# Kernel optimization log

Measured on AMD Instinct MI355X. Metric: run time of the kernel, lower is better.

Reference implementation:

```python
import jax, jax.numpy as jnp
import numpy as np

B, H, W, C = 32, 512, 512, 3


def setup_inputs() -> dict:
    key = jax.random.key(0)
    k1, k2, k3 = jax.random.split(key, 3)
    images = jax.random.normal(k1, (B, H, W, C), dtype=jnp.float32)
    # focal lengths in pixels, positive and well-conditioned
    focal = 400.0 + 200.0 * jax.random.uniform(k2, (B, 2), dtype=jnp.float32)
    # quaternion ~ identity rotation + small noise (stddev=0.01), q0 mean 1
    q = jnp.array([1.0, 0.0, 0.0, 0.0], jnp.float32) + 0.01 * jax.random.normal(k3, (4,), dtype=jnp.float32)
    return {"images": images, "focal": focal, "q": q}


def _quaternion_to_R(q):
    # matches tf_quaternion_to_R: normalize so sum(q^2)=2, then outer product
    q = q * jnp.sqrt(2.0 / jnp.sum(q * q))
    Q = q[:, None] * q[None, :]  # [4,4], Q[i,j] = q_i q_j
    return jnp.array([
        [1.0 - Q[2, 2] - Q[3, 3], Q[1, 2] - Q[3, 0], Q[1, 3] + Q[2, 0]],
        [Q[1, 2] + Q[3, 0], 1.0 - Q[1, 1] - Q[3, 3], Q[2, 3] - Q[1, 0]],
        [Q[1, 3] - Q[2, 0], Q[2, 3] + Q[1, 0], 1.0 - Q[1, 1] - Q[2, 2]],
    ])


def _forward(images, focal, q):
    R = _quaternion_to_R(q)  # [3,3]
    d = jnp.concatenate([focal, jnp.ones((focal.shape[0], 1), focal.dtype)], axis=1)  # [B,3]
    # H = K @ R @ inv(K) with K = diag(d):  H[b,i,j] = d[b,i] * R[i,j] / d[b,j]
    Hm = R[None, :, :] * d[:, :, None] / d[:, None, :]  # [B,3,3]

    origin_x = jnp.float32(W / 2)
    origin_y = jnp.float32(H / 2)
    xs = jnp.arange(W, dtype=jnp.float32) - origin_x  # [W]
    ys = jnp.arange(H, dtype=jnp.float32) - origin_y  # [H]
    x, y = jnp.meshgrid(xs, ys)  # [H,W] each
    ps = jnp.stack([x.ravel(), y.ravel(), jnp.ones(H * W, jnp.float32)], axis=0)  # [3,N]

    ps_w = jnp.einsum('bij,jn->bin', Hm, ps)  # [B,3,N]
    x_w = (ps_w[:, 0, :] / ps_w[:, 2, :]).reshape(-1, H, W) + origin_x  # [B,H,W]
    y_w = (ps_w[:, 1, :] / ps_w[:, 2, :]).reshape(-1, H, W) + origin_y  # [B,H,W]

    # bilinear resampler (tf.contrib.resampler): zero outside image bounds
    x0 = jnp.floor(x_w)
    y0 = jnp.floor(y_w)
    wx = x_w - x0
    wy = y_w - y0
    x0i = x0.astype(jnp.int32)
    y0i = y0.astype(jnp.int32)

    b = jnp.arange(images.shape[0])[:, None, None]

    def corner(yi, xi, w):
        valid = (xi >= 0) & (xi <= W - 1) & (yi >= 0) & (yi <= H - 1)
        g = images[b, jnp.clip(yi, 0, H - 1), jnp.clip(xi, 0, W - 1)]  # [B,H,W,C]
        return g * (w * valid.astype(images.dtype))[..., None]

    out = (corner(y0i, x0i, (1.0 - wx) * (1.0 - wy))
           + corner(y0i, x0i + 1, wx * (1.0 - wy))
           + corner(y0i + 1, x0i, (1.0 - wx) * wy)
           + corner(y0i + 1, x0i + 1, wx * wy))
    return out


def reference(images, focal, q):
    return _forward(images, focal, q)
```

## Files before the change

### kernel.cpp

```cpp
#include <hip/hip_runtime.h>
#include <hip/hip_bf16.h>


#define IMG_H 512
#define IMG_W 512
#define IMG_C 3
#define NB    32

typedef float f32x4  __attribute__((ext_vector_type(4)));
typedef float f32x4u __attribute__((ext_vector_type(4), aligned(4)));
typedef float f32x2u __attribute__((ext_vector_type(2), aligned(4)));

__global__ __launch_bounds__(256) void warp_kernel(
    const float* __restrict__ images,
    const float* __restrict__ focal,
    const float* __restrict__ q,
    float* __restrict__ out)
{
    const unsigned bid  = blockIdx.x;
    const unsigned xcd  = bid & 7u;
    const unsigned slot = bid >> 3;
    const unsigned virt = xcd * 2048u + slot;
    const int b = (int)(virt >> 9);
    const int y = (int)(virt & 511u);

    const int tid = threadIdx.x;

    __shared__ float sH[9];
    __shared__ float s_out[IMG_W * IMG_C];

    if (tid == 0) {
        float q0 = q[0], q1 = q[1], q2 = q[2], q3 = q[3];
        float s = sqrtf(2.0f / (q0*q0 + q1*q1 + q2*q2 + q3*q3));
        q0 *= s; q1 *= s; q2 *= s; q3 *= s;
        float R00 = 1.0f - q2*q2 - q3*q3;
        float R01 = q1*q2 - q3*q0;
        float R02 = q1*q3 + q2*q0;
        float R10 = q1*q2 + q3*q0;
        float R11 = 1.0f - q1*q1 - q3*q3;
        float R12 = q2*q3 - q1*q0;
        float R20 = q1*q3 - q2*q0;
        float R21 = q2*q3 + q1*q0;
        float R22 = 1.0f - q1*q1 - q2*q2;
        float d0 = focal[b*2 + 0];
        float d1 = focal[b*2 + 1];
        sH[0] = (R00*d0)/d0; sH[1] = (R01*d0)/d1; sH[2] = (R02*d0);
        sH[3] = (R10*d1)/d0; sH[4] = (R11*d1)/d1; sH[5] = (R12*d1);
        sH[6] = R20/d0;      sH[7] = R21/d1;      sH[8] = R22;
    }
    __syncthreads();

    const float h0 = sH[0], h3 = sH[3], h6 = sH[6];

    const float ys = (float)y - 256.0f;
    const float r1 = sH[1]*ys + sH[2];
    const float r4 = sH[4]*ys + sH[5];
    const float r7 = sH[7]*ys + sH[8];

    const float* __restrict__ img_b = images + (unsigned)b * (IMG_H * IMG_W * IMG_C);

    #define SAMPLE(PX, A0, A1, A2) do {                                        \
        const float xs = (float)(PX) - 256.0f;                                 \
        float p0 = fmaf(h0, xs, r1);                                           \
        float p1 = fmaf(h3, xs, r4);                                           \
        float p2 = fmaf(h6, xs, r7);                                           \
        float rp2 = __builtin_amdgcn_rcpf(p2);                                 \
        float xw = fmaf(p0, rp2, 256.0f);                                      \
        float yw = fmaf(p1, rp2, 256.0f);                                      \
        float x0f = floorf(xw), y0f = floorf(yw);                              \
        float wx = xw - x0f,   wy = yw - y0f;                                  \
        int x0 = (int)x0f, y0i = (int)y0f;                                     \
        bool interior = (x0 >= 0) & (y0i >= 0) &                               \
                        (x0 < IMG_W-1) & (y0i < IMG_H-1);                      \
        if (__all(interior)) {                                                 \
             \
            const float* bpA = img_b + ((unsigned)y0i * IMG_W + (unsigned)x0) * 3u; \
            const float* bpB = bpA + IMG_W * 3u;                               \
            f32x4u vA0 = *reinterpret_cast<const f32x4u*>(bpA);                \
            f32x2u vA1 = *reinterpret_cast<const f32x2u*>(bpA + 4);            \
            f32x4u vB0 = *reinterpret_cast<const f32x4u*>(bpB);                \
            f32x2u vB1 = *reinterpret_cast<const f32x2u*>(bpB + 4);            \
            float w00 = (1.0f - wx) * (1.0f - wy);                             \
            float w01 = wx * (1.0f - wy);                                      \
            float w10 = (1.0f - wx) * wy;                                      \
            float w11 = wx * wy;                                               \
            A0 = vA0.x*w00 + vA0.w*w01 + vB0.x*w10 + vB0.w*w11;                \
            A1 = vA0.y*w00 + vA1.x*w01 + vB0.y*w10 + vB1.x*w11;                \
            A2 = vA0.z*w00 + vA1.y*w01 + vB0.z*w10 + vB1.y*w11;                \
        } else {                                                               \
                     \
            int x1 = x0 + 1, y1i = y0i + 1;                                    \
            bool vx0 = (x0 >= 0) & (x0 <= IMG_W-1);                            \
            bool vx1 = (x1 >= 0) & (x1 <= IMG_W-1);                            \
            bool vy0 = (y0i >= 0) & (y0i <= IMG_H-1);                          \
            bool vy1 = (y1i >= 0) & (y1i <= IMG_H-1);                          \
            unsigned xc0 = (unsigned)min(max(x0, 0), IMG_W-1);                 \
            unsigned xc1 = (unsigned)min(max(x1, 0), IMG_W-1);                 \
            unsigned yc0 = (unsigned)min(max(y0i, 0), IMG_H-1);                \
            unsigned yc1 = (unsigned)min(max(y1i, 0), IMG_H-1);                \
            const float* p00 = img_b + (yc0 * IMG_W + xc0) * IMG_C;            \
            const float* p01 = img_b + (yc0 * IMG_W + xc1) * IMG_C;            \
            const float* p10 = img_b + (yc1 * IMG_W + xc0) * IMG_C;            \
            const float* p11 = img_b + (yc1 * IMG_W + xc1) * IMG_C;            \
            float a00 = p00[0], a01 = p00[1], a02 = p00[2];                    \
            float b00 = p01[0], b01 = p01[1], b02 = p01[2];                    \
            float c00 = p10[0], c01 = p10[1], c02 = p10[2];                    \
            float d00 = p11[0], d01 = p11[1], d02 = p11[2];                    \
            float w00 = (vx0 & vy0) ? (1.0f - wx) * (1.0f - wy) : 0.0f;        \
            float w01 = (vx1 & vy0) ? wx * (1.0f - wy)          : 0.0f;        \
            float w10 = (vx0 & vy1) ? (1.0f - wx) * wy          : 0.0f;        \
            float w11 = (vx1 & vy1) ? wx * wy                   : 0.0f;        \
            A0 = a00*w00 + b00*w01 + c00*w10 + d00*w11;                        \
            A1 = a01*w00 + b01*w01 + c01*w10 + d01*w11;                        \
            A2 = a02*w00 + b02*w01 + c02*w10 + d02*w11;                        \
        }                                                                      \
    } while (0)

    float o0a, o1a, o2a, o0b, o1b, o2b;
    SAMPLE(tid,        o0a, o1a, o2a);
    SAMPLE(tid + 256,  o0b, o1b, o2b);
    #undef SAMPLE

    s_out[tid*3 + 0] = o0a;
    s_out[tid*3 + 1] = o1a;
    s_out[tid*3 + 2] = o2a;
    s_out[(tid + 256)*3 + 0] = o0b;
    s_out[(tid + 256)*3 + 1] = o1b;
    s_out[(tid + 256)*3 + 2] = o2b;
    __syncthreads();

    f32x4* outp = reinterpret_cast<f32x4*>(
        out + ((unsigned)(b * IMG_H + y)) * (IMG_W * IMG_C));
    f32x4 v0 = *reinterpret_cast<const f32x4*>(&s_out[tid * 4]);
    __builtin_nontemporal_store(v0, &outp[tid]);
    if (tid < 128) {
        f32x4 v1 = *reinterpret_cast<const f32x4*>(&s_out[(256 + tid) * 4]);
        __builtin_nontemporal_store(v1, &outp[256 + tid]);
    }
}

extern "C" void kernel_launch(void* const* d_in, const int* in_sizes, int n_in,
                              void* d_out, int out_size, void* d_ws, size_t ws_size,
                              hipStream_t stream) {
    const float* images = (const float*)d_in[0];
    const float* focal  = (const float*)d_in[1];
    const float* q      = (const float*)d_in[2];
    float* out = (float*)d_out;

    dim3 grid(16384);
    dim3 block(256);
    warp_kernel<<<grid, block, 0, stream>>>(images, focal, q, out);
}
```

Measured before the change: 33.55 us.

## Compute homography per thread and store adjacent pixel pairs directly without LDS

```diff
diff --git a/kernel.cpp b/kernel.cpp
--- a/kernel.cpp
+++ b/kernel.cpp
@@ -7,7 +7,6 @@
 #define IMG_C 3
 #define NB    32
 
-typedef float f32x4  __attribute__((ext_vector_type(4)));
 typedef float f32x4u __attribute__((ext_vector_type(4), aligned(4)));
 typedef float f32x2u __attribute__((ext_vector_type(2), aligned(4)));
 
@@ -26,36 +25,37 @@
 
     const int tid = threadIdx.x;
 
-    __shared__ float sH[9];
-    __shared__ float s_out[IMG_W * IMG_C];
-
-    if (tid == 0) {
-        float q0 = q[0], q1 = q[1], q2 = q[2], q3 = q[3];
+    float q0 = q[0], q1 = q[1], q2 = q[2], q3 = q[3];
+    {
         float s = sqrtf(2.0f / (q0*q0 + q1*q1 + q2*q2 + q3*q3));
         q0 *= s; q1 *= s; q2 *= s; q3 *= s;
-        float R00 = 1.0f - q2*q2 - q3*q3;
-        float R01 = q1*q2 - q3*q0;
-        float R02 = q1*q3 + q2*q0;
-        float R10 = q1*q2 + q3*q0;
-        float R11 = 1.0f - q1*q1 - q3*q3;
-        float R12 = q2*q3 - q1*q0;
-        float R20 = q1*q3 - q2*q0;
-        float R21 = q2*q3 + q1*q0;
-        float R22 = 1.0f - q1*q1 - q2*q2;
-        float d0 = focal[b*2 + 0];
-        float d1 = focal[b*2 + 1];
-        sH[0] = (R00*d0)/d0; sH[1] = (R01*d0)/d1; sH[2] = (R02*d0);
-        sH[3] = (R10*d1)/d0; sH[4] = (R11*d1)/d1; sH[5] = (R12*d1);
-        sH[6] = R20/d0;      sH[7] = R21/d1;      sH[8] = R22;
     }
-    __syncthreads();
+    const float R00 = 1.0f - q2*q2 - q3*q3;
+    const float R01 = q1*q2 - q3*q0;
+    const float R02 = q1*q3 + q2*q0;
+    const float R10 = q1*q2 + q3*q0;
+    const float R11 = 1.0f - q1*q1 - q3*q3;
+    const float R12 = q2*q3 - q1*q0;
+    const float R20 = q1*q3 - q2*q0;
+    const float R21 = q2*q3 + q1*q0;
+    const float R22 = 1.0f - q1*q1 - q2*q2;
+    const float d0 = focal[b*2 + 0];
+    const float d1 = focal[b*2 + 1];
 
-    const float h0 = sH[0], h3 = sH[3], h6 = sH[6];
+    const float h0 = (R00*d0)/d0;
+    const float h1 = (R01*d0)/d1;
+    const float h2 = (R02*d0);
+    const float h3 = (R10*d1)/d0;
+    const float h4 = (R11*d1)/d1;
+    const float h5 = (R12*d1);
+    const float h6 = R20/d0;
+    const float h7 = R21/d1;
+    const float h8 = R22;
 
     const float ys = (float)y - 256.0f;
-    const float r1 = sH[1]*ys + sH[2];
-    const float r4 = sH[4]*ys + sH[5];
-    const float r7 = sH[7]*ys + sH[8];
+    const float r1 = h1*ys + h2;
+    const float r4 = h4*ys + h5;
+    const float r7 = h7*ys + h8;
 
     const float* __restrict__ img_b = images + (unsigned)b * (IMG_H * IMG_W * IMG_C);
 
@@ -88,7 +88,7 @@
             A1 = vA0.y*w00 + vA1.x*w01 + vB0.y*w10 + vB1.x*w11;                \
             A2 = vA0.z*w00 + vA1.y*w01 + vB0.z*w10 + vB1.y*w11;                \
         } else {                                                               \
-                     \
+                          \
             int x1 = x0 + 1, y1i = y0i + 1;                                    \
             bool vx0 = (x0 >= 0) & (x0 <= IMG_W-1);                            \
             bool vx1 = (x1 >= 0) & (x1 <= IMG_W-1);                            \
@@ -116,27 +116,17 @@
         }                                                                      \
     } while (0)
 
+    const int px = tid * 2;
     float o0a, o1a, o2a, o0b, o1b, o2b;
-    SAMPLE(tid,        o0a, o1a, o2a);
-    SAMPLE(tid + 256,  o0b, o1b, o2b);
+    SAMPLE(px,     o0a, o1a, o2a);
+    SAMPLE(px + 1, o0b, o1b, o2b);
     #undef SAMPLE
 
-    s_out[tid*3 + 0] = o0a;
-    s_out[tid*3 + 1] = o1a;
-    s_out[tid*3 + 2] = o2a;
-    s_out[(tid + 256)*3 + 0] = o0b;
-    s_out[(tid + 256)*3 + 1] = o1b;
-    s_out[(tid + 256)*3 + 2] = o2b;
-    __syncthreads();
-
-    f32x4* outp = reinterpret_cast<f32x4*>(
-        out + ((unsigned)(b * IMG_H + y)) * (IMG_W * IMG_C));
-    f32x4 v0 = *reinterpret_cast<const f32x4*>(&s_out[tid * 4]);
-    __builtin_nontemporal_store(v0, &outp[tid]);
-    if (tid < 128) {
-        f32x4 v1 = *reinterpret_cast<const f32x4*>(&s_out[(256 + tid) * 4]);
-        __builtin_nontemporal_store(v1, &outp[256 + tid]);
-    }
+    float* outp = out + ((unsigned)(b * IMG_H + y)) * (IMG_W * IMG_C) + (unsigned)px * 3u;
+    f32x4u s0; s0.x = o0a; s0.y = o1a; s0.z = o2a; s0.w = o0b;
+    f32x2u s1; s1.x = o1b; s1.y = o2b;
+    __builtin_nontemporal_store(s0, reinterpret_cast<f32x4u*>(outp));
+    __builtin_nontemporal_store(s1, reinterpret_cast<f32x2u*>(outp + 4));
 }
 
 extern "C" void kernel_launch(void* const* d_in, const int* in_sizes, int n_in,
```

Measured after the change: 38.92 us. 1.16x slower.
